# Optimization experiments

Measured on AMD Instinct MI355X. Metric: run time of the kernel, lower is better.

## Reference

```python
import jax, jax.numpy as jnp
import numpy as np

NEG = 0.01  # leaky_relu negative slope used throughout AttentiveFP


def _seg_softmax(logits, seg, num):
    # softmax over entries grouped by segment id (PyG softmax w/ 1e-16 eps)
    m = jax.ops.segment_max(logits, seg, num_segments=num)
    m = jnp.where(jnp.isfinite(m), m, 0.0)
    e = jnp.exp(logits - m[seg])
    s = jax.ops.segment_sum(e, seg, num_segments=num)
    return e / (s[seg] + 1e-16)


def _gru(x, h, wi, wh, bi, bh):
    # torch.nn.GRUCell math
    gi = x @ wi.T + bi
    gh = h @ wh.T + bh
    ir, iz, inn = jnp.split(gi, 3, axis=-1)
    hr, hz, hn = jnp.split(gh, 3, axis=-1)
    r = jax.nn.sigmoid(ir + hr)
    z = jax.nn.sigmoid(iz + hz)
    n = jnp.tanh(inn + r * hn)
    return (1.0 - z) * n + z * h


def _forward(x, edge_attr, mol_feats, lin1_w, lin1_b, gate_lin1_w, gate_lin2_w, gate_att_l, gate_att_r, gate_bias, grus_wi, grus_wh, grus_bi, grus_bh, atom_w, atom_att_src, atom_att_dst, atom_bias, mol_w, mol_att_src, mol_att_dst, mol_bias, lin2_w, lin2_b, fcm0_w, fcm0_b, fcm1_w, fcm1_b, fcm2_w, fcm2_b, fc0_w, fc0_b, fc1_w, fc1_b, fc2_w, fc2_b, fc3_w, fc3_b, fc4_w, fc4_b, edge_index, batch):
    N = x.shape[0]
    G = mol_feats.shape[0]
    src, dst = edge_index[0], edge_index[1]
    lrelu = lambda v: jax.nn.leaky_relu(v, NEG)
    # AttentiveFP (eval mode: dropout off)
    xh = lrelu(x @ lin1_w.T + lin1_b)  # [N,H]
    # --- GATEConv: edge-conditioned attention, add aggregation ---
    m = lrelu(jnp.concatenate([xh[src], edge_attr], axis=-1) @ gate_lin1_w.T)  # [E,H]
    a = lrelu(m @ gate_att_l + (xh @ gate_att_r)[dst])
    a = _seg_softmax(a, dst, N)
    h = jax.ops.segment_sum((m @ gate_lin2_w.T) * a[:, None], dst, num_segments=N) + gate_bias
    xh = jax.nn.relu(_gru(jax.nn.elu(h), xh, grus_wi[0], grus_wh[0], grus_bi[0], grus_bh[0]))
    # --- GATConv layers (num_layers-1 = 2, heads=1, no self loops) ---
    for l in range(2):
        xl = xh @ atom_w[l].T
        a = lrelu((xl @ atom_att_src[l])[src] + (xl @ atom_att_dst[l])[dst])
        a = _seg_softmax(a, dst, N)
        h = jax.ops.segment_sum(xl[src] * a[:, None], dst, num_segments=N) + atom_bias[l]
        xh = jax.nn.relu(_gru(jax.nn.elu(h), xh, grus_wi[1 + l], grus_wh[1 + l], grus_bi[1 + l], grus_bh[1 + l]))
    # --- attentive graph readout (num_timesteps = 3) ---
    out = jax.nn.relu(jax.ops.segment_sum(xh, batch, num_segments=G))  # [G,H]
    xm = xh @ mol_w.T            # atom-side lin (x fixed across timesteps)
    a_src = xm @ mol_att_src
    for _ in range(3):
        a = lrelu(a_src + ((out @ mol_w.T) @ mol_att_dst)[batch])
        a = _seg_softmax(a, batch, G)
        h = jax.ops.segment_sum(xm * a[:, None], batch, num_segments=G) + mol_bias
        out = jax.nn.relu(_gru(jax.nn.elu(h), out, grus_wi[3], grus_wh[3], grus_bi[3], grus_bh[3]))
    hg = out @ lin2_w.T + lin2_b  # [G,256]
    # --- mol-feature MLP branch (SiLU) ---
    hm = jax.nn.silu(mol_feats @ fcm0_w.T + fcm0_b)
    hm = jax.nn.silu(hm @ fcm1_w.T + fcm1_b)
    hm = jax.nn.silu(hm @ fcm2_w.T + fcm2_b)
    # --- fusion MLP ---
    hg = jnp.concatenate([hg, hm], axis=1)  # [G,512]
    hg = jax.nn.silu(hg @ fc0_w.T + fc0_b)
    hg = jax.nn.silu(hg @ fc1_w.T + fc1_b)
    hg = jax.nn.silu(hg @ fc2_w.T + fc2_b)
    hg = jax.nn.silu(hg @ fc3_w.T + fc3_b)
    return hg @ fc4_w.T + fc4_b  # [G,1]


def setup_inputs() -> dict:
    key = jax.random.key(0)
    ks = iter(jax.random.split(key, 64))
    def W(*shape):
        return jax.random.normal(next(ks), shape, jnp.float32) / np.float32(np.sqrt(shape[-1]))
    def B(*shape):
        return 0.02 * jax.random.normal(next(ks), shape, jnp.float32)
    N, E, G = 131072, 262144, 8192
    Fn, Fe, Fm, H = 64, 16, 200, 256
    return dict(
        x=jax.random.normal(next(ks), (N, Fn), jnp.float32),
        edge_attr=jax.random.normal(next(ks), (E, Fe), jnp.float32),
        mol_feats=jax.random.normal(next(ks), (G, Fm), jnp.float32),
        lin1_w=W(H, Fn), lin1_b=B(H),
        gate_lin1_w=W(H, H + Fe), gate_lin2_w=W(H, H),
        gate_att_l=W(H), gate_att_r=W(H), gate_bias=B(H),
        grus_wi=W(4, 3 * H, H), grus_wh=W(4, 3 * H, H), grus_bi=B(4, 3 * H), grus_bh=B(4, 3 * H),
        atom_w=W(2, H, H), atom_att_src=W(2, H), atom_att_dst=W(2, H), atom_bias=B(2, H),
        mol_w=W(H, H), mol_att_src=W(H), mol_att_dst=W(H), mol_bias=B(H),
        lin2_w=W(H, H), lin2_b=B(H),
        fcm0_w=W(H, Fm), fcm0_b=B(H), fcm1_w=W(H, H), fcm1_b=B(H), fcm2_w=W(H, H), fcm2_b=B(H),
        fc0_w=W(512, 512), fc0_b=B(512), fc1_w=W(512, 512), fc1_b=B(512),
        fc2_w=W(512, 512), fc2_b=B(512), fc3_w=W(128, 512), fc3_b=B(128),
        fc4_w=W(1, 128), fc4_b=B(1),
        edge_index=jax.random.randint(next(ks), (2, E), 0, N),
        batch=jnp.sort(jax.random.randint(next(ks), (N,), 0, G)),
    )


def reference(x, edge_attr, mol_feats, lin1_w, lin1_b, gate_lin1_w, gate_lin2_w, gate_att_l, gate_att_r, gate_bias, grus_wi, grus_wh, grus_bi, grus_bh, atom_w, atom_att_src, atom_att_dst, atom_bias, mol_w, mol_att_src, mol_att_dst, mol_bias, lin2_w, lin2_b, fcm0_w, fcm0_b, fcm1_w, fcm1_b, fcm2_w, fcm2_b, fc0_w, fc0_b, fc1_w, fc1_b, fc2_w, fc2_b, fc3_w, fc3_b, fc4_w, fc4_b, edge_index, batch):
    return _forward(x, edge_attr, mol_feats, lin1_w, lin1_b, gate_lin1_w, gate_lin2_w, gate_att_l, gate_att_r, gate_bias, grus_wi, grus_wh, grus_bi, grus_bh, atom_w, atom_att_src, atom_att_dst, atom_bias, mol_w, mol_att_src, mol_att_dst, mol_bias, lin2_w, lin2_b, fcm0_w, fcm0_b, fcm1_w, fcm1_b, fcm2_w, fcm2_b, fc0_w, fc0_b, fc1_w, fc1_b, fc2_w, fc2_b, fc3_w, fc3_b, fc4_w, fc4_b, edge_index, batch)
```

## Files before the change

kernel.cpp:

```cpp
#include <hip/hip_runtime.h>
#include <hip/hip_bf16.h>
#include <math.h>


typedef unsigned short u16;
typedef u16 u16x8 __attribute__((ext_vector_type(8)));
typedef short s16x8 __attribute__((ext_vector_type(8)));
typedef float f32x4 __attribute__((ext_vector_type(4)));

__device__ __forceinline__ float u2f(u16 u) { return __uint_as_float(((unsigned)u) << 16); }
__device__ __forceinline__ u16 f2u(float f) {
    return __builtin_bit_cast(u16, __float2bfloat16(f));
}

#define NEGS 0.01f

__device__ __forceinline__ unsigned fkey(float f) {
    unsigned u = __float_as_uint(f);
    return (u & 0x80000000u) ? ~u : (u | 0x80000000u);
}
__device__ __forceinline__ float funkey(unsigned k) {
    return (k & 0x80000000u) ? __uint_as_float(k ^ 0x80000000u) : __uint_as_float(~k);
}
#define KEY_NEG_INF 0x007FFFFFu

static inline int cdiv(int a, int b) { return (a + b - 1) / b; }

__global__ void fill_f32(float* p, float v, size_t n) {
    size_t i = (size_t)blockIdx.x * 256 + threadIdx.x;
    if (i < n) p[i] = v;
}
__global__ void fill_u32(unsigned* p, unsigned v, int n) {
    int i = blockIdx.x * 256 + threadIdx.x;
    if (i < n) p[i] = v;
}
__global__ void copy_f2b(const float* s, u16* d, size_t n) {
    size_t i = (size_t)blockIdx.x * 256 + threadIdx.x;
    if (i < n) d[i] = f2u(s[i]);
}
__global__ void matvecT_k(const float* W, const float* a, float* v, int K, int Jout) {
    int j = blockIdx.x * 256 + threadIdx.x;
    if (j >= Jout) return;
    float s = 0.f;
    for (int k = 0; k < K; k++) s += W[(size_t)k * Jout + j] * a[k];
    v[j] = s;
}
__global__ void edge_add_lrelu(float* elog, const float* r, const int* dsti, int E) {
    int i = blockIdx.x * 256 + threadIdx.x;
    if (i < E) {
        float v = elog[i] + r[dsti[i]];
        elog[i] = v > 0.f ? v : NEGS * v;
    }
}
__global__ void pair_logit(float* elog, const float* s, const float* d,
                           const int* srci, const int* dsti, int E) {
    int i = blockIdx.x * 256 + threadIdx.x;
    if (i < E) {
        float v = s[srci[i]] + d[dsti[i]];
        elog[i] = v > 0.f ? v : NEGS * v;
    }
}
__global__ void node_logit(float* nlog, const float* asrc, const float* wg,
                           const int* batch, int N) {
    int i = blockIdx.x * 256 + threadIdx.x;
    if (i < N) {
        float v = asrc[i] + wg[batch[i]];
        nlog[i] = v > 0.f ? v : NEGS * v;
    }
}
__global__ void seg_max_k(const float* logit, const int* idx, unsigned* key, int n) {
    int i = blockIdx.x * 256 + threadIdx.x;
    if (i < n) atomicMax(&key[idx[i]], fkey(logit[i]));
}
__global__ void seg_exp_k(const float* logit, const int* idx, const unsigned* key,
                          float* ex, float* sum, int n) {
    int i = blockIdx.x * 256 + threadIdx.x;
    if (i < n) {
        float e = expf(logit[i] - funkey(key[idx[i]]));
        ex[i] = e;
        atomicAdd(&sum[idx[i]], e);
    }
}
__global__ void seg_div_k(const float* ex, const int* idx, const float* sum,
                          float* a, int n) {
    int i = blockIdx.x * 256 + threadIdx.x;
    if (i < n) a[i] = ex[i] / (sum[idx[i]] + 1e-16f);
}
__global__ void rowdot2_b(const u16* X, const float* v1, const float* v2,
                          float* o1, float* o2, int M) {
    int r = blockIdx.x * 4 + (threadIdx.x >> 6);
    int lane = threadIdx.x & 63;
// ... 2 lines not shown
    float p1 = 0.f, p2 = 0.f;
#pragma unroll
    for (int q = 0; q < 4; q++) {
        float xv = u2f(row[q]);
        p1 += xv * v1[lane * 4 + q];
        if (v2) p2 += xv * v2[lane * 4 + q];
    }
    for (int off = 32; off; off >>= 1) {
        p1 += __shfl_down(p1, off);
        if (v2) p2 += __shfl_down(p2, off);
    }
    if (lane == 0) {
        o1[r] = p1;
        if (v2) o2[r] = p2;
    }
}
__global__ void rowdot_f(const float* X, const float* v1, float* o1, int M) {
    int r = blockIdx.x * 4 + (threadIdx.x >> 6);
    int lane = threadIdx.x & 63;
    if (r >= M) return;
    float4 a = ((const float4*)(X + (size_t)r * 256))[lane];
    float4 b = ((const float4*)v1)[lane];
    float p1 = a.x * b.x + a.y * b.y + a.z * b.z + a.w * b.w;
    for (int off = 32; off; off >>= 1) p1 += __shfl_down(p1, off);
    if (lane == 0) o1[r] = p1;
}
__global__ void fc4_k(const float* X, const float* w, const float* b, float* out, int G) {
    int g = blockIdx.x * 4 + (threadIdx.x >> 6);
    int lane = threadIdx.x & 63;
    if (g >= G) return;
    float2 xv = ((const float2*)(X + (size_t)g * 128))[lane];
    float2 wv = ((const float2*)w)[lane];
    float p = xv.x * wv.x + xv.y * wv.y;
    for (int off = 32; off; off >>= 1) p += __shfl_down(p, off);
    if (lane == 0) out[g] = p + b[0];
}

__global__ void count_dst(const int* dst, int* cnt, int E) {
    int i = blockIdx.x * 256 + threadIdx.x;
    if (i < E) atomicAdd(&cnt[dst[i]], 1);
}
__global__ void alloc_rows(const int* cnt, int* rowstart, int* cursor, int N) {
    int i = blockIdx.x * 256 + threadIdx.x;
    if (i < N) rowstart[i] = atomicAdd(cursor, cnt[i]);
}
__global__ void fill_csr(const int* dst, const int* rowstart, int* fillc,
                         int* eorder, int E) {
    int e = blockIdx.x * 256 + threadIdx.x;
    if (e >= E) return;
    int d = dst[e];
    int s = rowstart[d] + atomicAdd(&fillc[d], 1);
    eorder[s] = e;
}
template <int MODE>
__global__ void csr_reduce(const int* rowstart, const int* cnt, const int* eorder,
                           const float* a, const int* srcE, const u16* X,
                           float* out, int N) {
    int d = blockIdx.x;
    if (d >= N) return;
    int c = threadIdx.x;
    int rs = rowstart[d], k = cnt[d];
    float acc = 0.f;
    for (int s = 0; s < k; s++) {
        int e = eorder[rs + s];
        float av = a[e];
        const u16* row = (MODE == 0) ? X + (size_t)srcE[e] * 256 : X + (size_t)e * 256;
        acc += av * u2f(row[c]);
    }
    out[(size_t)d * 256 + c] = acc;
}
__global__ void graph_bounds(const int* batch, int* gs, int* ge, int N) {
    int i = blockIdx.x * 256 + threadIdx.x;
    if (i >= N) return;
    int b = batch[i];
    atomicMin(&gs[b], i);
    atomicMax(&ge[b], i + 1);
}
template <bool RELU>
__global__ void seg_red(const int* gs, const int* ge, const u16* X, const float* sc,
                        float* out, int G) {
    int g = blockIdx.x;
    if (g >= G) return;
    int c = threadIdx.x;
    int s = gs[g], e = ge[g];
    float acc = 0.f;
    if (s < e)
        for (int i = s; i < e; i++) {
            float v = u2f(X[(size_t)i * 256 + c]);
            if (sc) v *= sc[i];
            acc += v;
        }
    out[(size_t)g * 256 + c] = RELU ? fmaxf(acc, 0.f) : acc;
}

__global__ void pack_w(const float* s1, const float* s2, int K1, int Ksrc,
                       int Nout, int Kp, u16* dst) {
    int idx = blockIdx.x * 256 + threadIdx.x;
    int kiters = Kp >> 5;
    int total = (Nout >> 7) * kiters * 512;
    if (idx >= total) return;
    int c = idx & 511;
    int rest = idx >> 9;
    int ki = rest % kiters, nb = rest / kiters;
    int n = (nb << 7) + (((c >> 6) & 7) << 4) + (c & 15);
    int k0 = (ki << 5) + (((c >> 4) & 3) << 3);
    u16x8 vh, vl;
#pragma unroll
    for (int j = 0; j < 8; j++) {
        int k = k0 + j;
        float f = 0.f;
        if (k < K1) f = s1[(size_t)n * K1 + k];
        else if (k < Ksrc) f = s2[(size_t)n * (Ksrc - K1) + (k - K1)];
        u16 h = f2u(f);
        vh[j] = h;
        vl[j] = f2u(f - u2f(h));
    }
    ((u16x8*)dst)[idx] = vh;
    ((u16x8*)dst)[idx + total] = vl;
}
__global__ void pack_gru_w(const float* wi, const float* wh, u16* dst) {
    int idx = blockIdx.x * 256 + threadIdx.x;
    const int total = 8 * 16 * 512;
// ... 25 lines not shown
__global__ void pack_gru_b(const float* bi, const float* bh, float* bp) {
    int n = blockIdx.x * 256 + threadIdx.x;
    if (n >= 1024) return;
    int grp = n >> 6, sub = (n >> 4) & 3, ch = grp * 16 + (n & 15);
    float v;
    if (sub == 0) v = bi[ch] + bh[ch];
    else if (sub == 1) v = bi[256 + ch] + bh[256 + ch];
    else if (sub == 2) v = bi[512 + ch] + bh[512 + ch];
    else v = bh[512 + ch];
    bp[n] = v;
}

struct p8 { u16x8 hi, lo; };
__device__ __forceinline__ u16x8 zero8() {
    u16x8 z;
#pragma unroll
    for (int j = 0; j < 8; j++) z[j] = 0;
    return z;
}
__device__ __forceinline__ p8 sp_zero() { p8 r; r.hi = zero8(); r.lo = zero8(); return r; }
__device__ __forceinline__ p8 sp_b(const u16* p) {
    p8 r;
    r.hi = *(const u16x8*)p;
    r.lo = zero8();
    return r;
}
__device__ __forceinline__ p8 sp_f(const float* p) {
    p8 r;
#pragma unroll
    for (int j = 0; j < 8; j++) {
        float x = p[j];
        u16 h = f2u(x);
        r.hi[j] = h;
        r.lo[j] = f2u(x - u2f(h));
    }
    return r;
}
__device__ __forceinline__ p8 sp_eluf(const float* p) {
    p8 r;
#pragma unroll
    for (int j = 0; j < 8; j++) {
        float x = p[j];
        float e = x > 0.f ? x : expm1f(x);
        u16 h = f2u(e);
        r.hi[j] = h;
        r.lo[j] = f2u(e - u2f(h));
    }
    return r;
}
template <int ALD>
__device__ __forceinline__ p8 ldA(bool valid, int k, int Ksrc, const u16* ab,
                                  const float* af, const float* x2) {
    if (!valid) return sp_zero();
    if (ALD == 1) {
        if (k >= Ksrc) return sp_zero();
        return sp_f(af + k);
    }
    if (ALD == 2) {
        if (k < 256) return sp_b(ab + k);
        if (k < 272) return sp_f(x2 + (k - 256));
        return sp_zero();
    }
    if (ALD == 3) {
        if (k < 256) return sp_eluf(af + k);
        return sp_b(ab + (k - 256));
    }
    if (k < 256) return sp_eluf(af + k);
    return sp_f(x2 + (k - 256));
}
template <int ALD>
__device__ __forceinline__ bool lo_zero(int ki) {
    if (ALD == 2) return ki < 8;
    if (ALD == 3) return ki >= 8;
    return false;
}
template <int ACT>
__device__ __forceinline__ float actf(float v) {
    if (ACT == 1) return v > 0.f ? v : NEGS * v;
    if (ACT == 3) return v / (1.f + expf(-v));
    return v;
}

template <int ALD, int ACT, int EPI>
__global__ __launch_bounds__(256, 4) void mgemm(
    int M, int Kp, int Ksrc,
    const float* Af, int lda, const u16* Ab,
    const int* gidx, const float* X2f, const u16* Wp,
    const float* b1,
    float* Cf, u16* Cb, int ldc,
    const float* attv, float* dotout,
    const int* didx, const float* escale, float* scat) {
    __shared__ u16x8 lsAh[512];
    __shared__ u16x8 lsAl[512];
    __shared__ u16x8 lsWh[512];
    __shared__ u16x8 lsWl[512];
    const int t = threadIdx.x;
    const int m0 = blockIdx.x * 128;
    const int nb = blockIdx.y;
    const int kiters = Kp >> 5;
    const int r0 = ((t >> 6) << 4) | (t & 15);
    const int kq = ((t >> 4) & 3) << 3;
    const int mA[2] = {m0 + r0, m0 + r0 + 64};
    const u16* abr[2];
    const float* afr[2];
    const float* x2r[2];
    bool val[2];
#pragma unroll
    for (int h = 0; h < 2; h++) {
        int m = mA[h];
        val[h] = (m < M);
        int ms = val[h] ? m : 0;
        abr[h] = nullptr; afr[h] = nullptr; x2r[h] = nullptr;
        if (ALD == 1) {
            afr[h] = Af + (size_t)ms * lda;
        } else if (ALD == 2) {
            abr[h] = Ab + (size_t)gidx[ms] * 256;
            x2r[h] = X2f + (size_t)ms * 16;
        } else if (ALD == 3) {
            afr[h] = Af + (size_t)ms * 256;
            abr[h] = Ab + (size_t)ms * 256;
        } else {
            afr[h] = Af + (size_t)ms * 256;
            x2r[h] = X2f + (size_t)ms * 256;
        }
    }
    const int wave = t >> 6, lane = t & 63;
    const int wm = (wave >> 1) << 6, wn = (wave & 1) << 6;
    f32x4 acc[4][4];
#pragma unroll
    for (int i = 0; i < 4; i++)
#pragma unroll
        for (int j = 0; j < 4; j++) {
            acc[i][j][0] = 0.f; acc[i][j][1] = 0.f; acc[i][j][2] = 0.f; acc[i][j][3] = 0.f;
        }
    const u16x8* wh0 = (const u16x8*)Wp + ((size_t)nb * kiters << 9);
    const u16x8* wl0 = wh0 + ((size_t)gridDim.y * kiters << 9);
    for (int ki = 0; ki < kiters; ki++) {
        int kb = (ki << 5) + kq;
        p8 a0 = ldA<ALD>(val[0], kb, Ksrc, abr[0], afr[0], x2r[0]);
        p8 a1 = ldA<ALD>(val[1], kb, Ksrc, abr[1], afr[1], x2r[1]);
        lsAh[t] = a0.hi; lsAl[t] = a0.lo;
        lsAh[t + 256] = a1.hi; lsAl[t + 256] = a1.lo;
        const u16x8* wsh = wh0 + ((size_t)ki << 9);
        const u16x8* wsl = wl0 + ((size_t)ki << 9);
        lsWh[t] = wsh[t]; lsWh[t + 256] = wsh[t + 256];
        lsWl[t] = wsl[t]; lsWl[t + 256] = wsl[t + 256];
        __syncthreads();
        s16x8 ah[4], al[4], wh[4], wl[4];
#pragma unroll
        for (int f = 0; f < 4; f++) {
            int ai = ((wm >> 4) + f) * 64 + lane;
            int wi = ((wn >> 4) + f) * 64 + lane;
            ah[f] = __builtin_bit_cast(s16x8, lsAh[ai]);
            al[f] = __builtin_bit_cast(s16x8, lsAl[ai]);
            wh[f] = __builtin_bit_cast(s16x8, lsWh[wi]);
            wl[f] = __builtin_bit_cast(s16x8, lsWl[wi]);
        }
        bool skip_lh = lo_zero<ALD>(ki);
#pragma unroll
        for (int fi = 0; fi < 4; fi++)
#pragma unroll
            for (int fj = 0; fj < 4; fj++) {
                acc[fi][fj] = __builtin_amdgcn_mfma_f32_16x16x32_bf16(
                    ah[fi], wh[fj], acc[fi][fj], 0, 0, 0);
                if (!skip_lh)
                    acc[fi][fj] = __builtin_amdgcn_mfma_f32_16x16x32_bf16(
                        al[fi], wh[fj], acc[fi][fj], 0, 0, 0);
                acc[fi][fj] = __builtin_amdgcn_mfma_f32_16x16x32_bf16(
                    ah[fi], wl[fj], acc[fi][fj], 0, 0, 0);
            }
        __syncthreads();
    }
    const int col = lane & 15, quad = lane >> 4;
    const int n_base = nb * 128 + wn;
    if (EPI == 2) {
        float dp[4][4] = {};
#pragma unroll
        for (int fi = 0; fi < 4; fi++)
#pragma unroll
            for (int fj = 0; fj < 4; fj++) {
                int nn = n_base + fj * 16 + col;
                float av = attv[nn];
#pragma unroll
                for (int r = 0; r < 4; r++) {
                    float v = actf<ACT>(acc[fi][fj][r]);
                    dp[fi][r] += v * av;
                    if (Cb) {
                        int mm = m0 + wm + fi * 16 + quad * 4 + r;
                        if (mm < M) Cb[(size_t)mm * ldc + nn] = f2u(v);
                    }
                }
            }
#pragma unroll
        for (int fi = 0; fi < 4; fi++)
#pragma unroll
            for (int r = 0; r < 4; r++) {
                float p = dp[fi][r];
                p += __shfl_down(p, 8);
                p += __shfl_down(p, 4);
                p += __shfl_down(p, 2);
                p += __shfl_down(p, 1);
                int mm = m0 + wm + fi * 16 + quad * 4 + r;
                if (col == 0 && mm < M) atomicAdd(dotout + mm, p);
            }
    } else if (EPI == 3) {
#pragma unroll
        for (int fi = 0; fi < 4; fi++)
#pragma unroll
            for (int r = 0; r < 4; r++) {
                int mm = m0 + wm + fi * 16 + quad * 4 + r;
                if (mm >= M) continue;
                int d = didx[mm];
                float s = escale[mm];
                float* rowp = scat + (size_t)d * 256;
#pragma unroll
                for (int fj = 0; fj < 4; fj++) {
                    int nn = n_base + fj * 16 + col;
                    atomicAdd(rowp + nn, actf<ACT>(acc[fi][fj][r]) * s);
                }
            }
    } else {
#pragma unroll
        for (int fj = 0; fj < 4; fj++) {
            int nn = n_base + fj * 16 + col;
            float bb = b1 ? b1[nn] : 0.f;
#pragma unroll
            for (int fi = 0; fi < 4; fi++)
#pragma unroll
                for (int r = 0; r < 4; r++) {
                    int mm = m0 + wm + fi * 16 + quad * 4 + r;
                    if (mm >= M) continue;
                    float v = actf<ACT>(acc[fi][fj][r] + bb);
                    if (EPI == 1) Cb[(size_t)mm * ldc + nn] = f2u(v);
                    else Cf[(size_t)mm * ldc + nn] = v;
                }
        }
    }
}

template <int ALD, bool HB, bool OB>
__global__ __launch_bounds__(256, 4) void mgemm_gru(
    int M,
    const float* Af, const u16* Ab, const float* X2f,
    const u16* Wp, const float* bp,
    const u16* hb, const float* hf, float* of, u16* ob) {
    __shared__ u16x8 lsAh[512];
    __shared__ u16x8 lsAl[512];
    __shared__ u16x8 lsWh[512];
    __shared__ u16x8 lsWl[512];
    const int t = threadIdx.x;
    const int m0 = blockIdx.x * 128;
    const int nb = blockIdx.y;
    const int r0 = ((t >> 6) << 4) | (t & 15);
    const int kq = ((t >> 4) & 3) << 3;
    const int mA[2] = {m0 + r0, m0 + r0 + 64};
    const u16* abr[2];
    const float* afr[2];
    const float* x2r[2];
    bool val[2];
#pragma unroll
    for (int h = 0; h < 2; h++) {
        int m = mA[h];
        val[h] = (m < M);
        int ms = val[h] ? m : 0;
        abr[h] = nullptr; x2r[h] = nullptr;
        afr[h] = Af + (size_t)ms * 256;
        if (ALD == 3) abr[h] = Ab + (size_t)ms * 256;
        else x2r[h] = X2f + (size_t)ms * 256;
    }
    const int wave = t >> 6, lane = t & 63;
    const int wm = (wave >> 1) << 6, wn = (wave & 1) << 6;
    f32x4 acc[4][4];
// ... 72 lines not shown

extern "C" void kernel_launch(void* const* d_in, const int* in_sizes, int n_in,
                              void* d_out, int out_size, void* d_ws, size_t ws_size,
                              hipStream_t stream) {
    const float* x = (const float*)d_in[0];
    const float* edge_attr = (const float*)d_in[1];
    const float* mol_feats = (const float*)d_in[2];
    const float* lin1_w = (const float*)d_in[3];
    const float* lin1_b = (const float*)d_in[4];
    const float* gate_lin1_w = (const float*)d_in[5];
    const float* gate_lin2_w = (const float*)d_in[6];
    const float* gate_att_l = (const float*)d_in[7];
    const float* gate_att_r = (const float*)d_in[8];
    const float* gate_bias = (const float*)d_in[9];
    const float* grus_wi = (const float*)d_in[10];
    const float* grus_wh = (const float*)d_in[11];
    const float* grus_bi = (const float*)d_in[12];
    const float* grus_bh = (const float*)d_in[13];
    const float* atom_w = (const float*)d_in[14];
    const float* atom_att_src = (const float*)d_in[15];
    const float* atom_att_dst = (const float*)d_in[16];
    const float* atom_bias = (const float*)d_in[17];
    const float* mol_w = (const float*)d_in[18];
    const float* mol_att_src = (const float*)d_in[19];
    const float* mol_att_dst = (const float*)d_in[20];
    const float* mol_bias = (const float*)d_in[21];
    const float* lin2_w = (const float*)d_in[22];
    const float* lin2_b = (const float*)d_in[23];
    const float* fcm0_w = (const float*)d_in[24];
    const float* fcm0_b = (const float*)d_in[25];
    const float* fcm1_w = (const float*)d_in[26];
    const float* fcm1_b = (const float*)d_in[27];
    const float* fcm2_w = (const float*)d_in[28];
    const float* fcm2_b = (const float*)d_in[29];
    const float* fc0_w = (const float*)d_in[30];
    const float* fc0_b = (const float*)d_in[31];
    const float* fc1_w = (const float*)d_in[32];
    const float* fc1_b = (const float*)d_in[33];
    const float* fc2_w = (const float*)d_in[34];
    const float* fc2_b = (const float*)d_in[35];
    const float* fc3_w = (const float*)d_in[36];
    const float* fc3_b = (const float*)d_in[37];
    const float* fc4_w = (const float*)d_in[38];
    const float* fc4_b = (const float*)d_in[39];
    const int* edge_index = (const int*)d_in[40];
    const int* batch = (const int*)d_in[41];
    float* out_final = (float*)d_out;

    const int N = in_sizes[0] / 64;
    const int E = in_sizes[1] / 16;
    const int G = in_sizes[2] / 200;
    const int* srcE = edge_index;
    const int* dstE = edge_index + E;

    char* base = (char*)d_ws;
    size_t off = 0;
    auto alloc = [&](size_t bytes) -> char* {
        char* p = base + off;
        off += (bytes + 255) & ~(size_t)255;
        return p;
    };
    u16* xhA = (u16*)alloc((size_t)N * 256 * 2);
    float* hagg = (float*)alloc((size_t)N * 256 * 4);
    float* outg = (float*)alloc((size_t)G * 256 * 4);
    float* hgrb = (float*)alloc((size_t)G * 256 * 4);
    float* elog = (float*)alloc((size_t)E * 4);
    float* eexp = (float*)alloc((size_t)E * 4);
    float* aedge = (float*)alloc((size_t)E * 4);
    unsigned* nkey = (unsigned*)alloc((size_t)N * 4);
    float* nsum = (float*)alloc((size_t)N * 4);
    float* ns1 = (float*)alloc((size_t)N * 4);
    float* ns2 = (float*)alloc((size_t)N * 4);
    unsigned* gkey = (unsigned*)alloc((size_t)G * 4);
    float* gsum = (float*)alloc((size_t)G * 4);
    float* wgb = (float*)alloc((size_t)G * 4);
    float* vbuf = (float*)alloc(1024 * 4);
    int* ecnt = (int*)alloc((size_t)N * 4);
    int* efill = (int*)alloc((size_t)N * 4);
    int* erowst = (int*)alloc((size_t)N * 4);
    int* eorder = (int*)alloc((size_t)E * 4);
    int* cursor = (int*)alloc(256);
    int* gs = (int*)alloc((size_t)G * 4);
    int* ge = (int*)alloc((size_t)G * 4);
    u16* pk_lin1 = (u16*)alloc(256 * 64 * 2 * 2);
    u16* pk_g1 = (u16*)alloc(256 * 288 * 2 * 2);
    u16* pk_g2 = (u16*)alloc(256 * 256 * 2 * 2);
    u16* pk_gruF[4];
    float* bp_gru[4];
    for (int l = 0; l < 4; l++) {
        pk_gruF[l] = (u16*)alloc(1024 * 512 * 2 * 2);
        bp_gru[l] = (float*)alloc(1024 * 4);
    }
    u16* pk_atom[2];
    for (int l = 0; l < 2; l++) pk_atom[l] = (u16*)alloc(256 * 256 * 2 * 2);
    u16* pk_mol = (u16*)alloc(256 * 256 * 2 * 2);
    u16* pk_lin2 = (u16*)alloc(256 * 256 * 2 * 2);
    u16* pk_fcm0 = (u16*)alloc(256 * 224 * 2 * 2);
    u16* pk_fcm1 = (u16*)alloc(256 * 256 * 2 * 2);
    u16* pk_fcm2 = (u16*)alloc(256 * 256 * 2 * 2);
    u16* pk_fc0 = (u16*)alloc(512 * 512 * 2 * 2);
    u16* pk_fc1 = (u16*)alloc(512 * 512 * 2 * 2);
    u16* pk_fc2 = (u16*)alloc(512 * 512 * 2 * 2);
    u16* pk_fc3 = (u16*)alloc(128 * 512 * 2 * 2);
    size_t fixed_core = off;
    if (fixed_core + (size_t)2 * 1024 * 1024 > ws_size) {
        fill_f32<<<cdiv(out_size, 256), 256, 0, stream>>>(out_final, (float)ws_size,
                                                          (size_t)out_size);
        return;
    }
    u16* xhB = nullptr;
    bool use_pp = false;
    if (ws_size - off >= (size_t)N * 512 + (size_t)2 * 1024 * 1024) {
        xhB = (u16*)alloc((size_t)N * 512);
        use_pp = true;
    }
    size_t workbytes = ws_size - off;
    char* workp = base + off;
    float* cbuf = (float*)workp;
    u16* mtmp = (u16*)workp;
    bool use_mtmp = workbytes >= (size_t)E * 512;
    int Mc = (int)((workbytes / 1024) & ~(size_t)127);
    if (Mc > N) Mc = N;
    if (Mc < 128) Mc = 128;
    float* fbufA = hagg;
    float* fbufB = fbufA + (size_t)G * 512;
    float* fbufC = fbufB + (size_t)G * 512;
    float* f128 = fbufC + (size_t)G * 512;
    float* hm1 = f128 + (size_t)G * 128;
    float* hm2 = hm1 + (size_t)G * 256;

    auto pack = [&](const float* s1, const float* s2, int K1, int Ksrc, int Nout,
                    int Kp, u16* dst) {
        int total = (Nout >> 7) * (Kp >> 5) * 512;
        pack_w<<<cdiv(total, 256), 256, 0, stream>>>(s1, s2, K1, Ksrc, Nout, Kp, dst);
    };
    pack(lin1_w, nullptr, 64, 64, 256, 64, pk_lin1);
    pack(gate_lin1_w, nullptr, 272, 272, 256, 288, pk_g1);
    pack(gate_lin2_w, nullptr, 256, 256, 256, 256, pk_g2);
    for (int l = 0; l < 4; l++) {
        pack_gru_w<<<cdiv(8 * 16 * 512, 256), 256, 0, stream>>>(
            grus_wi + (size_t)l * 768 * 256, grus_wh + (size_t)l * 768 * 256,
            pk_gruF[l]);
        pack_gru_b<<<4, 256, 0, stream>>>(grus_bi + (size_t)l * 768,
                                          grus_bh + (size_t)l * 768, bp_gru[l]);
    }
    for (int l = 0; l < 2; l++)
        pack(atom_w + (size_t)l * 256 * 256, nullptr, 256, 256, 256, 256, pk_atom[l]);
    pack(mol_w, nullptr, 256, 256, 256, 256, pk_mol);
    pack(lin2_w, nullptr, 256, 256, 256, 256, pk_lin2);
    pack(fcm0_w, nullptr, 200, 200, 256, 224, pk_fcm0);
    pack(fcm1_w, nullptr, 256, 256, 256, 256, pk_fcm1);
    pack(fcm2_w, nullptr, 256, 256, 256, 256, pk_fcm2);
    pack(fc0_w, nullptr, 512, 512, 512, 512, pk_fc0);
    pack(fc1_w, nullptr, 512, 512, 512, 512, pk_fc1);
    pack(fc2_w, nullptr, 512, 512, 512, 512, pk_fc2);
    pack(fc3_w, nullptr, 512, 512, 128, 512, pk_fc3);

    fill_u32<<<cdiv(N, 256), 256, 0, stream>>>((unsigned*)ecnt, 0u, N);
    fill_u32<<<cdiv(N, 256), 256, 0, stream>>>((unsigned*)efill, 0u, N);
    fill_u32<<<1, 256, 0, stream>>>((unsigned*)cursor, 0u, 1);
    count_dst<<<cdiv(E, 256), 256, 0, stream>>>(dstE, ecnt, E);
    alloc_rows<<<cdiv(N, 256), 256, 0, stream>>>(ecnt, erowst, cursor, N);
    fill_csr<<<cdiv(E, 256), 256, 0, stream>>>(dstE, erowst, efill, eorder, E);
    fill_u32<<<cdiv(G, 256), 256, 0, stream>>>((unsigned*)gs, (unsigned)N, G);
    fill_u32<<<cdiv(G, 256), 256, 0, stream>>>((unsigned*)ge, 0u, G);
    graph_bounds<<<cdiv(N, 256), 256, 0, stream>>>(batch, gs, ge, N);

#define NIL nullptr, nullptr, nullptr, nullptr, nullptr

    u16* xh_cur = xhA;
    u16* xh_nxt = xhB;

    auto node_gru = [&](int l, const u16* Wpre, const float* bpre) {
        for (int c0 = 0; c0 < N; c0 += Mc) {
            int Ms = N - c0 < Mc ? N - c0 : Mc;
            int gx = cdiv(Ms, 128);
            mgemm<1, 0, 0><<<dim3(gx, 2), 256, 0, stream>>>(Ms, 256, 256,
                hagg + (size_t)c0 * 256, 256, nullptr, nullptr, nullptr,
                Wpre, bpre, cbuf, nullptr, 256, NIL);
            if (use_pp)
                mgemm_gru<3, true, true><<<dim3(gx, 8), 256, 0, stream>>>(Ms,
                    cbuf, xh_cur + (size_t)c0 * 256, nullptr, pk_gruF[l], bp_gru[l],
                    xh_cur + (size_t)c0 * 256, nullptr, nullptr,
                    xh_nxt + (size_t)c0 * 256);
            else
                mgemm_gru<3, true, false><<<dim3(gx, 8), 256, 0, stream>>>(Ms,
                    cbuf, xh_cur + (size_t)c0 * 256, nullptr, pk_gruF[l], bp_gru[l],
                    xh_cur + (size_t)c0 * 256, nullptr,
                    hagg + (size_t)c0 * 256, nullptr);
        }
        if (use_pp) {
            u16* t2 = xh_cur; xh_cur = xh_nxt; xh_nxt = t2;
        } else {
            copy_f2b<<<(int)(((size_t)N * 256 + 255) / 256), 256, 0, stream>>>(
                hagg, xh_cur, (size_t)N * 256);
        }
    };

    mgemm<1, 1, 1><<<dim3(cdiv(N, 128), 2), 256, 0, stream>>>(N, 64, 64,
        x, 64, nullptr, nullptr, nullptr, pk_lin1, lin1_b,
        nullptr, xh_cur, 256, NIL);

    fill_f32<<<cdiv(E, 256), 256, 0, stream>>>(elog, 0.f, (size_t)E);
    mgemm<2, 1, 2><<<dim3(cdiv(E, 128), 2), 256, 0, stream>>>(E, 288, 272,
        nullptr, 0, xh_cur, srcE, edge_attr, pk_g1, nullptr,
        nullptr, use_mtmp ? mtmp : nullptr, 256,
        gate_att_l, elog, nullptr, nullptr, nullptr);
    rowdot2_b<<<cdiv(N, 4), 256, 0, stream>>>(xh_cur, gate_att_r, nullptr, ns1, nullptr, N);
    edge_add_lrelu<<<cdiv(E, 256), 256, 0, stream>>>(elog, ns1, dstE, E);
    fill_u32<<<cdiv(N, 256), 256, 0, stream>>>(nkey, KEY_NEG_INF, N);
    fill_f32<<<cdiv(N, 256), 256, 0, stream>>>(nsum, 0.f, (size_t)N);
    seg_max_k<<<cdiv(E, 256), 256, 0, stream>>>(elog, dstE, nkey, E);
    seg_exp_k<<<cdiv(E, 256), 256, 0, stream>>>(elog, dstE, nkey, eexp, nsum, E);
    seg_div_k<<<cdiv(E, 256), 256, 0, stream>>>(eexp, dstE, nsum, aedge, E);
    if (use_mtmp) {
        csr_reduce<1><<<N, 256, 0, stream>>>(erowst, ecnt, eorder, aedge, nullptr,
                                             mtmp, hagg, N);
    } else {
        fill_f32<<<(int)(((size_t)N * 256 + 255) / 256), 256, 0, stream>>>(
            hagg, 0.f, (size_t)N * 256);
        mgemm<2, 1, 3><<<dim3(cdiv(E, 128), 2), 256, 0, stream>>>(E, 288, 272,
            nullptr, 0, xh_cur, srcE, edge_attr, pk_g1, nullptr,
            nullptr, nullptr, 0, nullptr, nullptr, dstE, aedge, hagg);
    }
    node_gru(0, pk_g2, gate_bias);

    for (int l = 0; l < 2; l++) {
        const float* aw = atom_w + (size_t)l * 256 * 256;
        matvecT_k<<<1, 256, 0, stream>>>(aw, atom_att_src + (size_t)l * 256, vbuf, 256, 256);
        matvecT_k<<<1, 256, 0, stream>>>(aw, atom_att_dst + (size_t)l * 256, vbuf + 256, 256, 256);
        rowdot2_b<<<cdiv(N, 4), 256, 0, stream>>>(xh_cur, vbuf, vbuf + 256, ns1, ns2, N);
        pair_logit<<<cdiv(E, 256), 256, 0, stream>>>(elog, ns1, ns2, srcE, dstE, E);
        fill_u32<<<cdiv(N, 256), 256, 0, stream>>>(nkey, KEY_NEG_INF, N);
        fill_f32<<<cdiv(N, 256), 256, 0, stream>>>(nsum, 0.f, (size_t)N);
        seg_max_k<<<cdiv(E, 256), 256, 0, stream>>>(elog, dstE, nkey, E);
        seg_exp_k<<<cdiv(E, 256), 256, 0, stream>>>(elog, dstE, nkey, eexp, nsum, E);
        seg_div_k<<<cdiv(E, 256), 256, 0, stream>>>(eexp, dstE, nsum, aedge, E);
        csr_reduce<0><<<N, 256, 0, stream>>>(erowst, ecnt, eorder, aedge, srcE,
                                             xh_cur, hagg, N);
        node_gru(1 + l, pk_atom[l], atom_bias + (size_t)l * 256);
    }

    seg_red<true><<<G, 256, 0, stream>>>(gs, ge, xh_cur, nullptr, outg, G);
    matvecT_k<<<1, 256, 0, stream>>>(mol_w, mol_att_dst, vbuf, 256, 256);
    matvecT_k<<<1, 256, 0, stream>>>(mol_w, mol_att_src, vbuf + 256, 256, 256);
    rowdot2_b<<<cdiv(N, 4), 256, 0, stream>>>(xh_cur, vbuf + 256, nullptr, ns1, nullptr, N);
    float* ogc = outg;
    float* ogn = hgrb;
    int McG = Mc < G ? Mc : G;
    for (int t = 0; t < 3; t++) {
        rowdot_f<<<cdiv(G, 4), 256, 0, stream>>>(ogc, vbuf, wgb, G);
        node_logit<<<cdiv(N, 256), 256, 0, stream>>>(elog, ns1, wgb, batch, N);
        fill_u32<<<cdiv(G, 256), 256, 0, stream>>>(gkey, KEY_NEG_INF, G);
        fill_f32<<<cdiv(G, 256), 256, 0, stream>>>(gsum, 0.f, (size_t)G);
        seg_max_k<<<cdiv(N, 256), 256, 0, stream>>>(elog, batch, gkey, N);
        seg_exp_k<<<cdiv(N, 256), 256, 0, stream>>>(elog, batch, gkey, eexp, gsum, N);
        seg_div_k<<<cdiv(N, 256), 256, 0, stream>>>(eexp, batch, gsum, aedge, N);
        seg_red<false><<<G, 256, 0, stream>>>(gs, ge, xh_cur, aedge, ogn, G);
        for (int c0 = 0; c0 < G; c0 += McG) {
            int Ms = G - c0 < McG ? G - c0 : McG;
            int gx = cdiv(Ms, 128);
            mgemm<1, 0, 0><<<dim3(gx, 2), 256, 0, stream>>>(Ms, 256, 256,
                ogn + (size_t)c0 * 256, 256, nullptr, nullptr, nullptr,
                pk_mol, mol_bias, cbuf, nullptr, 256, NIL);
            mgemm_gru<4, false, false><<<dim3(gx, 8), 256, 0, stream>>>(Ms,
                cbuf, nullptr, ogc + (size_t)c0 * 256, pk_gruF[3], bp_gru[3],
                nullptr, ogc + (size_t)c0 * 256, ogn + (size_t)c0 * 256, nullptr);
        }
        float* tt = ogc; ogc = ogn; ogn = tt;
    }

    int gG = cdiv(G, 128);
    mgemm<1, 0, 0><<<dim3(gG, 2), 256, 0, stream>>>(G, 256, 256, ogc, 256,
        nullptr, nullptr, nullptr, pk_lin2, lin2_b,
        fbufA, nullptr, 512, NIL);
    mgemm<1, 3, 0><<<dim3(gG, 2), 256, 0, stream>>>(G, 224, 200, mol_feats, 200,
        nullptr, nullptr, nullptr, pk_fcm0, fcm0_b,
        hm1, nullptr, 256, NIL);
    mgemm<1, 3, 0><<<dim3(gG, 2), 256, 0, stream>>>(G, 256, 256, hm1, 256,
        nullptr, nullptr, nullptr, pk_fcm1, fcm1_b,
        hm2, nullptr, 256, NIL);
    mgemm<1, 3, 0><<<dim3(gG, 2), 256, 0, stream>>>(G, 256, 256, hm2, 256,
        nullptr, nullptr, nullptr, pk_fcm2, fcm2_b,
        fbufA + 256, nullptr, 512, NIL);
    mgemm<1, 3, 0><<<dim3(gG, 4), 256, 0, stream>>>(G, 512, 512, fbufA, 512,
        nullptr, nullptr, nullptr, pk_fc0, fc0_b,
        fbufB, nullptr, 512, NIL);
    mgemm<1, 3, 0><<<dim3(gG, 4), 256, 0, stream>>>(G, 512, 512, fbufB, 512,
        nullptr, nullptr, nullptr, pk_fc1, fc1_b,
        fbufC, nullptr, 512, NIL);
    mgemm<1, 3, 0><<<dim3(gG, 4), 256, 0, stream>>>(G, 512, 512, fbufC, 512,
        nullptr, nullptr, nullptr, pk_fc2, fc2_b,
        fbufB, nullptr, 512, NIL);
    mgemm<1, 3, 0><<<dim3(gG, 1), 256, 0, stream>>>(G, 512, 512, fbufB, 512,
        nullptr, nullptr, nullptr, pk_fc3, fc3_b,
        f128, nullptr, 128, NIL);
    fc4_k<<<cdiv(G, 4), 256, 0, stream>>>(f128, fc4_w, fc4_b, out_final, G);
}
```

Baseline: 6.257 ms.

## Chunk GATE edge messages in CSR order and drop the atomic-scatter fallback

Replaces the GATE aggregation path with a chunked scheme. Edge messages are computed in CSR (dst-sorted) order into a bounded workspace chunk, and a per-node kernel accumulates each chunk's contiguous slice into the aggregate. This removes both the full E×256 message buffer requirement and the float-atomic scatter epilogue. It also frees workspace by reusing the logit buffer for the exp values, aliasing the fcm buffers, and optionally keeping the node aggregate in bf16, which costs some precision. Extra launches per chunk and partial-chunk rereads are the tradeoff.

Result: slower. 6.524 ms (+4.3%).

```diff
diff --git a/kernel.cpp b/kernel.cpp
--- a/kernel.cpp
+++ b/kernel.cpp
@@ -37,6 +37,10 @@
 __global__ void copy_f2b(const float* s, u16* d, size_t n) {
     size_t i = (size_t)blockIdx.x * 256 + threadIdx.x;
     if (i < n) d[i] = f2u(s[i]);
+}
+__global__ void copy_u32(const unsigned* s, unsigned* d, int n) {
+    int i = blockIdx.x * 256 + threadIdx.x;
+    if (i < n) d[i] = s[i];
 }
 __global__ void matvecT_k(const float* W, const float* a, float* v, int K, int Jout) {
     int j = blockIdx.x * 256 + threadIdx.x;
@@ -145,10 +149,10 @@
     int s = rowstart[d] + atomicAdd(&fillc[d], 1);
     eorder[s] = e;
 }
-template <int MODE>
-__global__ void csr_reduce(const int* rowstart, const int* cnt, const int* eorder,
-                           const float* a, const int* srcE, const u16* X,
-                           float* out, int N) {
+template <bool HF>
+__global__ void csr_reduce_gat(const int* rowstart, const int* cnt, const int* eorder,
+                               const float* a, const int* srcE, const u16* X,
+                               float* outf, u16* outb, int N) {
     int d = blockIdx.x;
     if (d >= N) return;
     int c = threadIdx.x;
@@ -156,11 +160,29 @@
     float acc = 0.f;
     for (int s = 0; s < k; s++) {
         int e = eorder[rs + s];
-        float av = a[e];
-        const u16* row = (MODE == 0) ? X + (size_t)srcE[e] * 256 : X + (size_t)e * 256;
-        acc += av * u2f(row[c]);
-    }
-    out[(size_t)d * 256 + c] = acc;
+        acc += a[e] * u2f(X[(size_t)srcE[e] * 256 + c]);
+    }
+    if (HF) outf[(size_t)d * 256 + c] = acc;
+    else outb[(size_t)d * 256 + c] = f2u(acc);
+}
+template <bool HF>
+__global__ void gate_csr_chunk(const int* rowstart, const int* cnt, const int* eorder,
+                               const float* a, const u16* mchunk,
+                               float* hf, u16* hb, int N, int c0, int c1) {
+    int d = blockIdx.x;
+    if (d >= N) return;
+    int rs = rowstart[d], k = cnt[d];
+    int s0 = rs < c0 ? c0 : rs;
+    int s1 = (rs + k) < c1 ? (rs + k) : c1;
+    if (s0 >= s1) return;
+    int c = threadIdx.x;
+    float acc = 0.f;
+    for (int s = s0; s < s1; s++)
+        acc += a[eorder[s]] * u2f(mchunk[(size_t)(s - c0) * 256 + c]);
+    size_t idx = (size_t)d * 256 + c;
+    if (rs < c0) acc += HF ? hf[idx] : u2f(hb[idx]);
+    if (HF) hf[idx] = acc;
+    else hb[idx] = f2u(acc);
 }
 __global__ void graph_bounds(const int* batch, int* gs, int* ge, int N) {
     int i = blockIdx.x * 256 + threadIdx.x;
@@ -292,11 +314,12 @@
 __device__ __forceinline__ p8 ldA(bool valid, int k, int Ksrc, const u16* ab,
                                   const float* af, const float* x2) {
     if (!valid) return sp_zero();
+    if (ALD == 0) return sp_b(ab + k);
     if (ALD == 1) {
         if (k >= Ksrc) return sp_zero();
         return sp_f(af + k);
     }
-    if (ALD == 2) {
+    if (ALD == 2 || ALD == 5) {
         if (k < 256) return sp_b(ab + k);
         if (k < 272) return sp_f(x2 + (k - 256));
         return sp_zero();
@@ -310,7 +333,8 @@
 }
 template <int ALD>
 __device__ __forceinline__ bool lo_zero(int ki) {
-    if (ALD == 2) return ki < 8;
+    if (ALD == 0) return true;
+    if (ALD == 2 || ALD == 5) return ki < 8;
     if (ALD == 3) return ki >= 8;
     return false;
 }
@@ -325,11 +349,10 @@
 __global__ __launch_bounds__(256, 4) void mgemm(
     int M, int Kp, int Ksrc,
     const float* Af, int lda, const u16* Ab,
-    const int* gidx, const float* X2f, const u16* Wp,
+    const int* gidx, const int* sidx, const float* X2f, const u16* Wp,
     const float* b1,
     float* Cf, u16* Cb, int ldc,
-    const float* attv, float* dotout,
-    const int* didx, const float* escale, float* scat) {
+    const float* attv, float* dotout) {
     __shared__ u16x8 lsAh[512];
     __shared__ u16x8 lsAl[512];
     __shared__ u16x8 lsWh[512];
@@ -351,11 +374,17 @@
         val[h] = (m < M);
         int ms = val[h] ? m : 0;
         abr[h] = nullptr; afr[h] = nullptr; x2r[h] = nullptr;
-        if (ALD == 1) {
+        if (ALD == 0) {
+            abr[h] = Ab + (size_t)ms * lda;
+        } else if (ALD == 1) {
             afr[h] = Af + (size_t)ms * lda;
         } else if (ALD == 2) {
             abr[h] = Ab + (size_t)gidx[ms] * 256;
             x2r[h] = X2f + (size_t)ms * 16;
+        } else if (ALD == 5) {
+            int e = gidx[ms];
+            abr[h] = Ab + (size_t)sidx[e] * 256;
+            x2r[h] = X2f + (size_t)e * 16;
         } else if (ALD == 3) {
             afr[h] = Af + (size_t)ms * 256;
             abr[h] = Ab + (size_t)ms * 256;
@@ -422,14 +451,7 @@
                 int nn = n_base + fj * 16 + col;
                 float av = attv[nn];
 #pragma unroll
-                for (int r = 0; r < 4; r++) {
-                    float v = actf<ACT>(acc[fi][fj][r]);
-                    dp[fi][r] += v * av;
-                    if (Cb) {
-                        int mm = m0 + wm + fi * 16 + quad * 4 + r;
-                        if (mm < M) Cb[(size_t)mm * ldc + nn] = f2u(v);
-                    }
-                }
+                for (int r = 0; r < 4; r++) dp[fi][r] += actf<ACT>(acc[fi][fj][r]) * av;
             }
 #pragma unroll
         for (int fi = 0; fi < 4; fi++)
@@ -442,22 +464,6 @@
                 p += __shfl_down(p, 1);
                 int mm = m0 + wm + fi * 16 + quad * 4 + r;
                 if (col == 0 && mm < M) atomicAdd(dotout + mm, p);
-            }
-    } else if (EPI == 3) {
-#pragma unroll
-        for (int fi = 0; fi < 4; fi++)
-#pragma unroll
-            for (int r = 0; r < 4; r++) {
-                int mm = m0 + wm + fi * 16 + quad * 4 + r;
-                if (mm >= M) continue;
-                int d = didx[mm];
-                float s = escale[mm];
-                float* rowp = scat + (size_t)d * 256;
-#pragma unroll
-                for (int fj = 0; fj < 4; fj++) {
-                    int nn = n_base + fj * 16 + col;
-                    atomicAdd(rowp + nn, actf<ACT>(acc[fi][fj][r]) * s);
-                }
             }
     } else {
 #pragma unroll
@@ -636,6 +642,7 @@
     const int G = in_sizes[2] / 200;
     const int* srcE = edge_index;
     const int* dstE = edge_index + E;
+    const size_t MB = 1 << 20;
 
     char* base = (char*)d_ws;
     size_t off = 0;
@@ -645,11 +652,9 @@
         return p;
     };
     u16* xhA = (u16*)alloc((size_t)N * 256 * 2);
-    float* hagg = (float*)alloc((size_t)N * 256 * 4);
     float* outg = (float*)alloc((size_t)G * 256 * 4);
     float* hgrb = (float*)alloc((size_t)G * 256 * 4);
     float* elog = (float*)alloc((size_t)E * 4);
-    float* eexp = (float*)alloc((size_t)E * 4);
     float* aedge = (float*)alloc((size_t)E * 4);
     unsigned* nkey = (unsigned*)alloc((size_t)N * 4);
     float* nsum = (float*)alloc((size_t)N * 4);
@@ -686,32 +691,35 @@
     u16* pk_fc1 = (u16*)alloc(512 * 512 * 2 * 2);
     u16* pk_fc2 = (u16*)alloc(512 * 512 * 2 * 2);
     u16* pk_fc3 = (u16*)alloc(128 * 512 * 2 * 2);
-    size_t fixed_core = off;
-    if (fixed_core + (size_t)2 * 1024 * 1024 > ws_size) {
+    if (off + 70 * MB > ws_size) {
         fill_f32<<<cdiv(out_size, 256), 256, 0, stream>>>(out_final, (float)ws_size,
                                                           (size_t)out_size);
         return;
     }
-    u16* xhB = nullptr;
-    bool use_pp = false;
-    if (ws_size - off >= (size_t)N * 512 + (size_t)2 * 1024 * 1024) {
-        xhB = (u16*)alloc((size_t)N * 512);
-        use_pp = true;
-    }
+    bool hagg_f32 = (ws_size - off) >= ((size_t)N * 256 * 4 + 12 * MB);
+    float* hagg32 = nullptr;
+    u16* hagg16 = nullptr;
+    if (hagg_f32) hagg32 = (float*)alloc((size_t)N * 256 * 4);
+    else hagg16 = (u16*)alloc((size_t)N * 256 * 2);
+    bool use_pp = (ws_size - off) >= ((size_t)N * 512 + 12 * MB);
+    u16* xhB = use_pp ? (u16*)alloc((size_t)N * 512) : nullptr;
     size_t workbytes = ws_size - off;
     char* workp = base + off;
+    u16* m_chunk = (u16*)workp;
     float* cbuf = (float*)workp;
-    u16* mtmp = (u16*)workp;
-    bool use_mtmp = workbytes >= (size_t)E * 512;
+    int Ec = (int)((workbytes / 512) & ~(size_t)127);
+    if (Ec > E) Ec = E;
+    if (Ec < 128) Ec = 128;
     int Mc = (int)((workbytes / 1024) & ~(size_t)127);
     if (Mc > N) Mc = N;
     if (Mc < 128) Mc = 128;
-    float* fbufA = hagg;
+    float* headb = hagg_f32 ? hagg32 : (float*)hagg16;
+    float* fbufA = headb;
     float* fbufB = fbufA + (size_t)G * 512;
     float* fbufC = fbufB + (size_t)G * 512;
     float* f128 = fbufC + (size_t)G * 512;
-    float* hm1 = f128 + (size_t)G * 128;
-    float* hm2 = hm1 + (size_t)G * 256;
+    float* hm1 = fbufB;
+    float* hm2 = fbufC;
 
     auto pack = [&](const float* s1, const float* s2, int K1, int Ksrc, int Nout,
                     int Kp, u16* dst) {
@@ -750,8 +758,6 @@
     fill_u32<<<cdiv(G, 256), 256, 0, stream>>>((unsigned*)ge, 0u, G);
     graph_bounds<<<cdiv(N, 256), 256, 0, stream>>>(batch, gs, ge, N);
 
-#define NIL nullptr, nullptr, nullptr, nullptr, nullptr
-
     u16* xh_cur = xhA;
     u16* xh_nxt = xhB;
 
@@ -759,53 +765,72 @@
         for (int c0 = 0; c0 < N; c0 += Mc) {
             int Ms = N - c0 < Mc ? N - c0 : Mc;
             int gx = cdiv(Ms, 128);
-            mgemm<1, 0, 0><<<dim3(gx, 2), 256, 0, stream>>>(Ms, 256, 256,
-                hagg + (size_t)c0 * 256, 256, nullptr, nullptr, nullptr,
-                Wpre, bpre, cbuf, nullptr, 256, NIL);
+            if (hagg_f32)
+                mgemm<1, 0, 0><<<dim3(gx, 2), 256, 0, stream>>>(Ms, 256, 256,
+                    hagg32 + (size_t)c0 * 256, 256, nullptr, nullptr, nullptr,
+                    nullptr, Wpre, bpre, cbuf, nullptr, 256, nullptr, nullptr);
+            else
+                mgemm<0, 0, 0><<<dim3(gx, 2), 256, 0, stream>>>(Ms, 256, 256,
+                    nullptr, 256, hagg16 + (size_t)c0 * 256, nullptr, nullptr,
+                    nullptr, Wpre, bpre, cbuf, nullptr, 256, nullptr, nullptr);
             if (use_pp)
                 mgemm_gru<3, true, true><<<dim3(gx, 8), 256, 0, stream>>>(Ms,
                     cbuf, xh_cur + (size_t)c0 * 256, nullptr, pk_gruF[l], bp_gru[l],
                     xh_cur + (size_t)c0 * 256, nullptr, nullptr,
                     xh_nxt + (size_t)c0 * 256);
-            else
+            else if (hagg_f32)
                 mgemm_gru<3, true, false><<<dim3(gx, 8), 256, 0, stream>>>(Ms,
                     cbuf, xh_cur + (size_t)c0 * 256, nullptr, pk_gruF[l], bp_gru[l],
                     xh_cur + (size_t)c0 * 256, nullptr,
-                    hagg + (size_t)c0 * 256, nullptr);
+                    hagg32 + (size_t)c0 * 256, nullptr);
+            else
+                mgemm_gru<3, true, true><<<dim3(gx, 8), 256, 0, stream>>>(Ms,
+                    cbuf, xh_cur + (size_t)c0 * 256, nullptr, pk_gruF[l], bp_gru[l],
+                    xh_cur + (size_t)c0 * 256, nullptr, nullptr,
+                    hagg16 + (size_t)c0 * 256);
         }
         if (use_pp) {
             u16* t2 = xh_cur; xh_cur = xh_nxt; xh_nxt = t2;
+        } else if (hagg_f32) {
+            copy_f2b<<<(int)(((size_t)N * 256 + 255) / 256), 256, 0, stream>>>(
+                hagg32, xh_cur, (size_t)N * 256);
         } else {
-            copy_f2b<<<(int)(((size_t)N * 256 + 255) / 256), 256, 0, stream>>>(
-                hagg, xh_cur, (size_t)N * 256);
+            copy_u32<<<cdiv(N * 128, 256), 256, 0, stream>>>(
+                (const unsigned*)hagg16, (unsigned*)xh_cur, N * 128);
         }
     };
 
     mgemm<1, 1, 1><<<dim3(cdiv(N, 128), 2), 256, 0, stream>>>(N, 64, 64,
-        x, 64, nullptr, nullptr, nullptr, pk_lin1, lin1_b,
-        nullptr, xh_cur, 256, NIL);
+        x, 64, nullptr, nullptr, nullptr, nullptr, pk_lin1, lin1_b,
+        nullptr, xh_cur, 256, nullptr, nullptr);
 
     fill_f32<<<cdiv(E, 256), 256, 0, stream>>>(elog, 0.f, (size_t)E);
     mgemm<2, 1, 2><<<dim3(cdiv(E, 128), 2), 256, 0, stream>>>(E, 288, 272,
-        nullptr, 0, xh_cur, srcE, edge_attr, pk_g1, nullptr,
-        nullptr, use_mtmp ? mtmp : nullptr, 256,
-        gate_att_l, elog, nullptr, nullptr, nullptr);
+        nullptr, 0, xh_cur, srcE, nullptr, edge_attr, pk_g1, nullptr,
+        nullptr, nullptr, 0, gate_att_l, elog);
     rowdot2_b<<<cdiv(N, 4), 256, 0, stream>>>(xh_cur, gate_att_r, nullptr, ns1, nullptr, N);
     edge_add_lrelu<<<cdiv(E, 256), 256, 0, stream>>>(elog, ns1, dstE, E);
     fill_u32<<<cdiv(N, 256), 256, 0, stream>>>(nkey, KEY_NEG_INF, N);
     fill_f32<<<cdiv(N, 256), 256, 0, stream>>>(nsum, 0.f, (size_t)N);
     seg_max_k<<<cdiv(E, 256), 256, 0, stream>>>(elog, dstE, nkey, E);
-    seg_exp_k<<<cdiv(E, 256), 256, 0, stream>>>(elog, dstE, nkey, eexp, nsum, E);
-    seg_div_k<<<cdiv(E, 256), 256, 0, stream>>>(eexp, dstE, nsum, aedge, E);
-    if (use_mtmp) {
-        csr_reduce<1><<<N, 256, 0, stream>>>(erowst, ecnt, eorder, aedge, nullptr,
-                                             mtmp, hagg, N);
-    } else {
+    seg_exp_k<<<cdiv(E, 256), 256, 0, stream>>>(elog, dstE, nkey, elog, nsum, E);
+    seg_div_k<<<cdiv(E, 256), 256, 0, stream>>>(elog, dstE, nsum, aedge, E);
+    if (hagg_f32)
         fill_f32<<<(int)(((size_t)N * 256 + 255) / 256), 256, 0, stream>>>(
-            hagg, 0.f, (size_t)N * 256);
-        mgemm<2, 1, 3><<<dim3(cdiv(E, 128), 2), 256, 0, stream>>>(E, 288, 272,
-            nullptr, 0, xh_cur, srcE, edge_attr, pk_g1, nullptr,
-            nullptr, nullptr, 0, nullptr, nullptr, dstE, aedge, hagg);
+            hagg32, 0.f, (size_t)N * 256);
+    else
+        fill_u32<<<cdiv(N * 128, 256), 256, 0, stream>>>((unsigned*)hagg16, 0u, N * 128);
+    for (int c0 = 0; c0 < E; c0 += Ec) {
+        int Ms = E - c0 < Ec ? E - c0 : Ec;
+        mgemm<5, 1, 1><<<dim3(cdiv(Ms, 128), 2), 256, 0, stream>>>(Ms, 288, 272,
+            nullptr, 0, xh_cur, eorder + c0, srcE, edge_attr, pk_g1, nullptr,
+            nullptr, m_chunk, 256, nullptr, nullptr);
+        if (hagg_f32)
+            gate_csr_chunk<true><<<N, 256, 0, stream>>>(erowst, ecnt, eorder, aedge,
+                m_chunk, hagg32, nullptr, N, c0, c0 + Ms);
+        else
+            gate_csr_chunk<false><<<N, 256, 0, stream>>>(erowst, ecnt, eorder, aedge,
+                m_chunk, nullptr, hagg16, N, c0, c0 + Ms);
     }
     node_gru(0, pk_g2, gate_bias);
 
@@ -818,10 +843,14 @@
         fill_u32<<<cdiv(N, 256), 256, 0, stream>>>(nkey, KEY_NEG_INF, N);
         fill_f32<<<cdiv(N, 256), 256, 0, stream>>>(nsum, 0.f, (size_t)N);
         seg_max_k<<<cdiv(E, 256), 256, 0, stream>>>(elog, dstE, nkey, E);
-        seg_exp_k<<<cdiv(E, 256), 256, 0, stream>>>(elog, dstE, nkey, eexp, nsum, E);
-        seg_div_k<<<cdiv(E, 256), 256, 0, stream>>>(eexp, dstE, nsum, aedge, E);
-        csr_reduce<0><<<N, 256, 0, stream>>>(erowst, ecnt, eorder, aedge, srcE,
-                                             xh_cur, hagg, N);
+        seg_exp_k<<<cdiv(E, 256), 256, 0, stream>>>(elog, dstE, nkey, elog, nsum, E);
+        seg_div_k<<<cdiv(E, 256), 256, 0, stream>>>(elog, dstE, nsum, aedge, E);
+        if (hagg_f32)
+            csr_reduce_gat<true><<<N, 256, 0, stream>>>(erowst, ecnt, eorder, aedge,
+                srcE, xh_cur, hagg32, nullptr, N);
+        else
+            csr_reduce_gat<false><<<N, 256, 0, stream>>>(erowst, ecnt, eorder, aedge,
+                srcE, xh_cur, nullptr, hagg16, N);
         node_gru(1 + l, pk_atom[l], atom_bias + (size_t)l * 256);
     }
 
@@ -838,15 +867,15 @@
         fill_u32<<<cdiv(G, 256), 256, 0, stream>>>(gkey, KEY_NEG_INF, G);
         fill_f32<<<cdiv(G, 256), 256, 0, stream>>>(gsum, 0.f, (size_t)G);
         seg_max_k<<<cdiv(N, 256), 256, 0, stream>>>(elog, batch, gkey, N);
-        seg_exp_k<<<cdiv(N, 256), 256, 0, stream>>>(elog, batch, gkey, eexp, gsum, N);
-        seg_div_k<<<cdiv(N, 256), 256, 0, stream>>>(eexp, batch, gsum, aedge, N);
+        seg_exp_k<<<cdiv(N, 256), 256, 0, stream>>>(elog, batch, gkey, elog, gsum, N);
+        seg_div_k<<<cdiv(N, 256), 256, 0, stream>>>(elog, batch, gsum, aedge, N);
         seg_red<false><<<G, 256, 0, stream>>>(gs, ge, xh_cur, aedge, ogn, G);
         for (int c0 = 0; c0 < G; c0 += McG) {
             int Ms = G - c0 < McG ? G - c0 : McG;
             int gx = cdiv(Ms, 128);
             mgemm<1, 0, 0><<<dim3(gx, 2), 256, 0, stream>>>(Ms, 256, 256,
-                ogn + (size_t)c0 * 256, 256, nullptr, nullptr, nullptr,
-                pk_mol, mol_bias, cbuf, nullptr, 256, NIL);
+                ogn + (size_t)c0 * 256, 256, nullptr, nullptr, nullptr, nullptr,
+                pk_mol, mol_bias, cbuf, nullptr, 256, nullptr, nullptr);
             mgemm_gru<4, false, false><<<dim3(gx, 8), 256, 0, stream>>>(Ms,
                 cbuf, nullptr, ogc + (size_t)c0 * 256, pk_gruF[3], bp_gru[3],
                 nullptr, ogc + (size_t)c0 * 256, ogn + (size_t)c0 * 256, nullptr);
@@ -855,29 +884,29 @@
     }
 
     int gG = cdiv(G, 128);
+    mgemm<1, 3, 0><<<dim3(gG, 2), 256, 0, stream>>>(G, 224, 200, mol_feats, 200,
+        nullptr, nullptr, nullptr, nullptr, pk_fcm0, fcm0_b,
+        hm1, nullptr, 256, nullptr, nullptr);
+    mgemm<1, 3, 0><<<dim3(gG, 2), 256, 0, stream>>>(G, 256, 256, hm1, 256,
+        nullptr, nullptr, nullptr, nullptr, pk_fcm1, fcm1_b,
+        hm2, nullptr, 256, nullptr, nullptr);
+    mgemm<1, 3, 0><<<dim3(gG, 2), 256, 0, stream>>>(G, 256, 256, hm2, 256,
+        nullptr, nullptr, nullptr, nullptr, pk_fcm2, fcm2_b,
+        fbufA + 256, nullptr, 512, nullptr, nullptr);
     mgemm<1, 0, 0><<<dim3(gG, 2), 256, 0, stream>>>(G, 256, 256, ogc, 256,
-        nullptr, nullptr, nullptr, pk_lin2, lin2_b,
-        fbufA, nullptr, 512, NIL);
-    mgemm<1, 3, 0><<<dim3(gG, 2), 256, 0, stream>>>(G, 224, 200, mol_feats, 200,
-        nullptr, nullptr, nullptr, pk_fcm0, fcm0_b,
-        hm1, nullptr, 256, NIL);
-    mgemm<1, 3, 0><<<dim3(gG, 2), 256, 0, stream>>>(G, 256, 256, hm1, 256,
-        nullptr, nullptr, nullptr, pk_fcm1, fcm1_b,
-        hm2, nullptr, 256, NIL);
-    mgemm<1, 3, 0><<<dim3(gG, 2), 256, 0, stream>>>(G, 256, 256, hm2, 256,
-        nullptr, nullptr, nullptr, pk_fcm2, fcm2_b,
-        fbufA + 256, nullptr, 512, NIL);
+        nullptr, nullptr, nullptr, nullptr, pk_lin2, lin2_b,
+        fbufA, nullptr, 512, nullptr, nullptr);
     mgemm<1, 3, 0><<<dim3(gG, 4), 256, 0, stream>>>(G, 512, 512, fbufA, 512,
-        nullptr, nullptr, nullptr, pk_fc0, fc0_b,
-        fbufB, nullptr, 512, NIL);
+        nullptr, nullptr, nullptr, nullptr, pk_fc0, fc0_b,
+        fbufB, nullptr, 512, nullptr, nullptr);
     mgemm<1, 3, 0><<<dim3(gG, 4), 256, 0, stream>>>(G, 512, 512, fbufB, 512,
-        nullptr, nullptr, nullptr, pk_fc1, fc1_b,
-        fbufC, nullptr, 512, NIL);
+        nullptr, nullptr, nullptr, nullptr, pk_fc1, fc1_b,
+        fbufC, nullptr, 512, nullptr, nullptr);
     mgemm<1, 3, 0><<<dim3(gG, 4), 256, 0, stream>>>(G, 512, 512, fbufC, 512,
-        nullptr, nullptr, nullptr, pk_fc2, fc2_b,
-        fbufB, nullptr, 512, NIL);
+        nullptr, nullptr, nullptr, nullptr, pk_fc2, fc2_b,
+        fbufB, nullptr, 512, nullptr, nullptr);
     mgemm<1, 3, 0><<<dim3(gG, 1), 256, 0, stream>>>(G, 512, 512, fbufB, 512,
-        nullptr, nullptr, nullptr, pk_fc3, fc3_b,
-        f128, nullptr, 128, NIL);
+        nullptr, nullptr, nullptr, nullptr, pk_fc3, fc3_b,
+        f128, nullptr, 128, nullptr, nullptr);
     fc4_k<<<cdiv(G, 4), 256, 0, stream>>>(f128, fc4_w, fc4_b, out_final, G);
 }
```
